# Kernel tuning notes

Hardware: AMD Instinct MI355X
Metric: run time of the kernel (lower is better)

The kernel has to match this reference:

```python
import jax, jax.numpy as jnp
import numpy as np

SRC_K = 11  # source neighborhood
GUI_K = 5   # guide neighborhood


def _unfold(x, k):
    # torch F.unfold(x, k, padding=k//2).view(B, C, k*k, H, W)
    # conv_general_dilated_patches (NCHW default) stacks patches channel-major:
    # output channels ordered (C, kh, kw), matching torch's view.
    p = jax.lax.conv_general_dilated_patches(x, (k, k), (1, 1), 'SAME')
    B, _, H, W = p.shape
    C = x.shape[1]
    return p.reshape(B, C, k * k, H, W)


def _conv1x1(x, w, b):
    # w: (Cout, Cin), 1x1 conv == per-pixel linear
    return jnp.einsum('oi,bihw->bohw', w, x) + b[None, :, None, None]


def setup_inputs() -> dict:
    key = jax.random.key(0)
    ks = jax.random.split(key, 6)
    B, C, H, W = 2, 64, 112, 112
    s1 = 1.0 / np.sqrt(C).astype(np.float32)
    s3 = 1.0 / np.sqrt(2 * C).astype(np.float32)
    return {
        'f_guide': jax.random.normal(ks[0], (B, C, H, W), jnp.float32),
        'f_source': jax.random.normal(ks[1], (B, C, H, W), jnp.float32),
        'w1': jax.random.normal(ks[2], (C, C), jnp.float32) * s1,
        'b1': jnp.zeros((C,), jnp.float32),
        'w2': jax.random.normal(ks[3], (C, C), jnp.float32) * s1,
        'b2': jnp.zeros((C,), jnp.float32),
        'w3': jax.random.normal(ks[4], (C, 2 * C), jnp.float32) * s3,
        'b3': jnp.zeros((C,), jnp.float32),
    }


def reference(f_guide, f_source, w1, b1, w2, b2, w3, b3):
    g = _conv1x1(f_guide, w1, b1)    # (B,C,H,W)
    s = _conv1x1(f_source, w2, b2)   # (B,C,H,W)

    # source -> guide: gather 11x11 source neighborhoods, score vs guide pixel
    fs = _unfold(s, SRC_K)                                   # (B,C,121,H,W)
    filt = jax.nn.softmax((fs * g[:, :, None]).sum(1), 1)    # (B,121,H,W)
    f_s2g = (fs * filt[:, None]).sum(2)                      # (B,C,H,W)

    # guide -> source: gather 5x5 guide neighborhoods, score vs source pixel
    fg = _unfold(g, GUI_K)                                   # (B,C,25,H,W)
    filt2 = jax.nn.softmax((fg * s[:, :, None]).sum(1), 1)   # (B,25,H,W)
    f_g2s = (fg * filt2[:, None]).sum(2)                     # (B,C,H,W)

    fusion = _conv1x1(jnp.concatenate([f_s2g, f_g2s], axis=1), w3, b3)
    return fusion
```

## Files before the change

### kernel.cpp

```cpp
#include <hip/hip_runtime.h>
#include <hip/hip_bf16.h>

constexpr int kH  = 112;
constexpr int kW  = 112;
constexpr int kC  = 64;
constexpr int kB  = 2;
constexpr int kHW = kH * kW;
constexpr int kNP = kB * kHW;

constexpr float kLog2e = 1.4426950408889634f;

__device__ __forceinline__ int xcd1568(int bid) { return (bid & 7) * 196 + (bid >> 3); }
__device__ __forceinline__ int xcd3136(int bid) { return (bid & 7) * 392 + (bid >> 3); }

__global__ __launch_bounds__(256)
void prep(const float* __restrict__ w1, const float* __restrict__ w2,
          const float* __restrict__ w3, float* __restrict__ w1t,
          float* __restrict__ w2t, float* __restrict__ w3t)
{
    const int idx = blockIdx.x * 256 + threadIdx.x;
    if (idx < 4096) {
        const int o = idx >> 6, c = idx & 63;
        w1t[c * 64 + o] = w1[idx];
    } else if (idx < 8192) {
        const int r = idx - 4096;
        const int o = r >> 6, c = r & 63;
        w2t[c * 64 + o] = w2[r];
    } else {
        const int r = idx - 8192;
        const int o = r >> 7, c = r & 127;
        w3t[c * 64 + o] = w3[r];
    }
}

__global__ __launch_bounds__(256, 4)
void conv_gs(const float* __restrict__ fg, const float* __restrict__ fs,
             const float* __restrict__ w1t, const float* __restrict__ b1,
             const float* __restrict__ w2t, const float* __restrict__ b2,
             float* __restrict__ gw, float* __restrict__ sw)
{
    __shared__ float wt[2][4096];
    __shared__ float xls[2][64 * 17];

    for (int idx = threadIdx.x; idx < 8192; idx += 256) {
        const int t = idx >> 12, rem = idx & 4095;
        wt[t][rem] = (t ? w2t : w1t)[rem];
    }

    const int d   = xcd1568(blockIdx.x);
    const int p0  = d * 16;
    const int b   = p0 / kHW;
    const int pb0 = p0 - b * kHW;

    for (int idx = threadIdx.x; idx < 2048; idx += 256) {
        const int t  = idx >> 10;
        const int c  = (idx >> 4) & 63;
        const int px = idx & 15;
        xls[t][c * 17 + px] = (t ? fs : fg)[(size_t)(b * kC + c) * kHW + pb0 + px];
    }
    __syncthreads();

    const int grp = threadIdx.x >> 4;
    const int i   = threadIdx.x & 15;
    const int t   = i >> 3;
    const int j   = i & 7;
    const int p   = p0 + grp;

    float x[8];
#pragma unroll
    for (int cc = 0; cc < 8; ++cc)
        x[cc] = xls[t][(8 * j + cc) * 17 + grp];

    const float* bias = t ? b2 : b1;
    const float* wts  = wt[t];

    float a[8];
    {
        const float4 bb0  = *(const float4*)(bias + 8 * j);
        const float4 bb1v = *(const float4*)(bias + 8 * j + 4);
        a[0] = bb0.x;  a[1] = bb0.y;  a[2] = bb0.z;  a[3] = bb0.w;
        a[4] = bb1v.x; a[5] = bb1v.y; a[6] = bb1v.z; a[7] = bb1v.w;
    }

    for (int c0 = 0; c0 < 64; c0 += 8) {
        const int sl = c0 >> 3;
#pragma unroll
        for (int k = 0; k < 8; ++k) {
            const float xc = __shfl(x[k], sl, 8);
            const float* wr = &wts[(c0 + k) * 64 + 8 * j];
            const float4 w0 = *(const float4*)(wr);
            const float4 w1v = *(const float4*)(wr + 4);
            a[0] = fmaf(w0.x, xc, a[0]);  a[1] = fmaf(w0.y, xc, a[1]);
            a[2] = fmaf(w0.z, xc, a[2]);  a[3] = fmaf(w0.w, xc, a[3]);
            a[4] = fmaf(w1v.x, xc, a[4]); a[5] = fmaf(w1v.y, xc, a[5]);
            a[6] = fmaf(w1v.z, xc, a[6]); a[7] = fmaf(w1v.w, xc, a[7]);
        }
    }
    float* dst = (t ? sw : gw) + (size_t)p * 64 + 8 * j;
    *(float4*)(dst)     = make_float4(a[0], a[1], a[2], a[3]);
    *(float4*)(dst + 4) = make_float4(a[4], a[5], a[6], a[7]);
}

template <int NN, int KD, int RAD, bool GUARD>
__device__ __forceinline__ void attn_phase(const float* __restrict__ base,
                                           const float qs[8], int pb, int h, int w,
                                           int t, int j, float acc[8], float& l)
{
    const float* np;
    bool v0 = true;
    {
        const int q = t / KD, r = t - q * KD;
        int off;
        if (GUARD) {
            const int hh = h + q - RAD, ww = w + r - RAD;
            v0 = ((unsigned)hh < (unsigned)kH) & ((unsigned)ww < (unsigned)kW);
            off = min(max(hh, 0), kH - 1) * kW + min(max(ww, 0), kW - 1);
        } else {
            off = pb + q * kW + r - (RAD * kW + RAD);
        }
        np = base + (size_t)off * 64 + 8 * j;
    }
    float4 n0 = *(const float4*)(np);
    float4 n1 = *(const float4*)(np + 4);

    for (int n = t; n < NN; n += 4) {
        float4 m0, m1;
        bool v1 = true;
        if (n + 4 < NN) {
            const int q = (n + 4) / KD, r = (n + 4) - q * KD;
            int off;
            if (GUARD) {
                const int hh = h + q - RAD, ww = w + r - RAD;
                v1 = ((unsigned)hh < (unsigned)kH) & ((unsigned)ww < (unsigned)kW);
                off = min(max(hh, 0), kH - 1) * kW + min(max(ww, 0), kW - 1);
            } else {
                off = pb + q * kW + r - (RAD * kW + RAD);
            }
            const float* np2 = base + (size_t)off * 64 + 8 * j;
            m0 = *(const float4*)(np2);
            m1 = *(const float4*)(np2 + 4);
        }

        float4 c0 = n0, c1 = n1;
        if (GUARD && !v0) {
            c0 = make_float4(0.f, 0.f, 0.f, 0.f);
            c1 = make_float4(0.f, 0.f, 0.f, 0.f);
        }
        float dd = c0.x * qs[0];
        dd = fmaf(c0.y, qs[1], dd);
        dd = fmaf(c0.z, qs[2], dd);
        dd = fmaf(c0.w, qs[3], dd);
        dd = fmaf(c1.x, qs[4], dd);
        dd = fmaf(c1.y, qs[5], dd);
        dd = fmaf(c1.z, qs[6], dd);
        dd = fmaf(c1.w, qs[7], dd);
        dd += __shfl_xor(dd, 1);
        dd += __shfl_xor(dd, 2);
        dd += __shfl_xor(dd, 4);
        const float pe = __builtin_amdgcn_exp2f(dd);
        l += pe;
        acc[0] = fmaf(pe, c0.x, acc[0]);
        acc[1] = fmaf(pe, c0.y, acc[1]);
        acc[2] = fmaf(pe, c0.z, acc[2]);
        acc[3] = fmaf(pe, c0.w, acc[3]);
        acc[4] = fmaf(pe, c1.x, acc[4]);
        acc[5] = fmaf(pe, c1.y, acc[5]);
        acc[6] = fmaf(pe, c1.z, acc[6]);
        acc[7] = fmaf(pe, c1.w, acc[7]);

        n0 = m0; n1 = m1; v0 = v1;
    }
}

__device__ __forceinline__ void merge4(float acc[8], float& l)
{
    l += __shfl_xor(l, 8);
    l += __shfl_xor(l, 16);
#pragma unroll
    for (int k = 0; k < 8; ++k) {
        acc[k] += __shfl_xor(acc[k], 8);
        acc[k] += __shfl_xor(acc[k], 16);
    }
}

__global__ __launch_bounds__(256, 8)
void attn_fuse(const float* __restrict__ gw, const float* __restrict__ sw,
               const float* __restrict__ w3t, const float* __restrict__ b3,
               float* __restrict__ out)
{
    const int d   = xcd3136(blockIdx.x);
    const int grp = threadIdx.x >> 5;
    const int i   = threadIdx.x & 31;
    const int t   = i >> 3;
    const int j   = i & 7;
    const int p   = d * 8 + grp;

    const int b  = p / kHW;
    const int pb = p - b * kHW;
    const int h  = pb / kW;
    const int w  = pb - h * kW;

    const float* gb = gw + (size_t)b * kHW * 64;
    const float* sb = sw + (size_t)b * kHW * 64;

    float fs2g[8];
    {
        float qs[8];
        const float4 g0 = *(const float4*)(gw + (size_t)p * 64 + 8 * j);
        const float4 g1 = *(const float4*)(gw + (size_t)p * 64 + 8 * j + 4);
        qs[0] = g0.x * kLog2e; qs[1] = g0.y * kLog2e;
        qs[2] = g0.z * kLog2e; qs[3] = g0.w * kLog2e;
        qs[4] = g1.x * kLog2e; qs[5] = g1.y * kLog2e;
        qs[6] = g1.z * kLog2e; qs[7] = g1.w * kLog2e;

        float acc[8] = {0.f, 0.f, 0.f, 0.f, 0.f, 0.f, 0.f, 0.f};
        float l = 0.f;
        if (h >= 5 && h < kH - 5 && w >= 5 && w < kW - 5)
            attn_phase<121, 11, 5, false>(sb, qs, pb, h, w, t, j, acc, l);
        else
            attn_phase<121, 11, 5, true>(sb, qs, pb, h, w, t, j, acc, l);
        merge4(acc, l);
        const float inv = 1.0f / l;
#pragma unroll
        for (int k = 0; k < 8; ++k) fs2g[k] = acc[k] * inv;
    }

    float fg2s[8];
    {
        float qs[8];
        const float4 s0 = *(const float4*)(sw + (size_t)p * 64 + 8 * j);
        const float4 s1 = *(const float4*)(sw + (size_t)p * 64 + 8 * j + 4);
        qs[0] = s0.x * kLog2e; qs[1] = s0.y * kLog2e;
        qs[2] = s0.z * kLog2e; qs[3] = s0.w * kLog2e;
        qs[4] = s1.x * kLog2e; qs[5] = s1.y * kLog2e;
        qs[6] = s1.z * kLog2e; qs[7] = s1.w * kLog2e;

        float acc[8] = {0.f, 0.f, 0.f, 0.f, 0.f, 0.f, 0.f, 0.f};
        float l = 0.f;
        if (h >= 2 && h < kH - 2 && w >= 2 && w < kW - 2)
            attn_phase<25, 5, 2, false>(gb, qs, pb, h, w, t, j, acc, l);
        else
            attn_phase<25, 5, 2, true>(gb, qs, pb, h, w, t, j, acc, l);
        merge4(acc, l);
        const float inv = 1.0f / l;
#pragma unroll
        for (int k = 0; k < 8; ++k) fg2s[k] = acc[k] * inv;
    }

    float xsrc[8];
#pragma unroll
    for (int k = 0; k < 8; ++k) xsrc[k] = (t < 2) ? fs2g[k] : fg2s[k];

    float fo[8] = {0.f, 0.f, 0.f, 0.f, 0.f, 0.f, 0.f, 0.f};
    for (int m0 = 0; m0 < 32; m0 += 8) {
        const int srcl = (((t & 1) << 5) + m0) >> 3;
        const float* wrow = w3t + (size_t)(t * 32 + m0) * 64 + 8 * j;
#pragma unroll
        for (int mm = 0; mm < 8; ++mm) {
            const float xc = __shfl(xsrc[mm], srcl, 8);
            const float4 w0 = *(const float4*)(wrow + mm * 64);
            const float4 w1v = *(const float4*)(wrow + mm * 64 + 4);
            fo[0] = fmaf(w0.x, xc, fo[0]);  fo[1] = fmaf(w0.y, xc, fo[1]);
            fo[2] = fmaf(w0.z, xc, fo[2]);  fo[3] = fmaf(w0.w, xc, fo[3]);
            fo[4] = fmaf(w1v.x, xc, fo[4]); fo[5] = fmaf(w1v.y, xc, fo[5]);
            fo[6] = fmaf(w1v.z, xc, fo[6]); fo[7] = fmaf(w1v.w, xc, fo[7]);
        }
    }
#pragma unroll
    for (int k = 0; k < 8; ++k) {
        fo[k] += __shfl_xor(fo[k], 8);
        fo[k] += __shfl_xor(fo[k], 16);
    }

    const float e0 = (t & 2) ? fo[4] : fo[0];
    const float e1 = (t & 2) ? fo[5] : fo[1];
    const float e2 = (t & 2) ? fo[6] : fo[2];
    const float e3 = (t & 2) ? fo[7] : fo[3];
    const float o0 = (t & 1) ? e2 : e0;
    const float o1 = (t & 1) ? e3 : e1;
    const int c0 = 8 * j + 2 * t;
    const size_t a0 = ((size_t)(b * kC + c0) * kH + h) * kW + w;
    out[a0]       = o0 + b3[c0];
    out[a0 + kHW] = o1 + b3[c0 + 1];
}

extern "C" void kernel_launch(void* const* d_in, const int* in_sizes, int n_in,
                              void* d_out, int out_size, void* d_ws, size_t ws_size,
                              hipStream_t stream)
{
    const float* fg = (const float*)d_in[0];
    const float* fs = (const float*)d_in[1];
    const float* w1 = (const float*)d_in[2];
    const float* b1 = (const float*)d_in[3];
    const float* w2 = (const float*)d_in[4];
    const float* b2 = (const float*)d_in[5];
    const float* w3 = (const float*)d_in[6];
    const float* b3 = (const float*)d_in[7];
    float* outp = (float*)d_out;

    float* gws = (float*)d_ws;
    float* sws = gws + (size_t)kNP * 64;
    float* w3t = sws + (size_t)kNP * 64;
    float* w1t = w3t + 128 * 64;
    float* w2t = w1t + 64 * 64;

    prep<<<64, 256, 0, stream>>>(w1, w2, w3, w1t, w2t, w3t);
    conv_gs<<<1568, 256, 0, stream>>>(fg, fs, w1t, b1, w2t, b2, gws, sws);
    attn_fuse<<<3136, 256, 0, stream>>>(gws, sws, w3t, b3, outp);
}
```

Before: 174.2 us.

## Stage attention neighborhoods in shared-memory tiles and read conv weights from global

```diff
diff --git a/kernel.cpp b/kernel.cpp
--- a/kernel.cpp
+++ b/kernel.cpp
@@ -11,7 +11,6 @@
 constexpr float kLog2e = 1.4426950408889634f;
 
 __device__ __forceinline__ int xcd1568(int bid) { return (bid & 7) * 196 + (bid >> 3); }
-__device__ __forceinline__ int xcd3136(int bid) { return (bid & 7) * 392 + (bid >> 3); }
 
 __global__ __launch_bounds__(256)
 void prep(const float* __restrict__ w1, const float* __restrict__ w2,
@@ -33,19 +32,13 @@
     }
 }
 
-__global__ __launch_bounds__(256, 4)
+__global__ __launch_bounds__(256, 6)
 void conv_gs(const float* __restrict__ fg, const float* __restrict__ fs,
              const float* __restrict__ w1t, const float* __restrict__ b1,
              const float* __restrict__ w2t, const float* __restrict__ b2,
              float* __restrict__ gw, float* __restrict__ sw)
 {
-    __shared__ float wt[2][4096];
     __shared__ float xls[2][64 * 17];
-
-    for (int idx = threadIdx.x; idx < 8192; idx += 256) {
-        const int t = idx >> 12, rem = idx & 4095;
-        wt[t][rem] = (t ? w2t : w1t)[rem];
-    }
 
     const int d   = xcd1568(blockIdx.x);
     const int p0  = d * 16;
@@ -72,7 +65,7 @@
         x[cc] = xls[t][(8 * j + cc) * 17 + grp];
 
     const float* bias = t ? b2 : b1;
-    const float* wts  = wt[t];
+    const float* wb   = t ? w2t : w1t;
 
     float a[8];
     {
@@ -87,7 +80,7 @@
 #pragma unroll
         for (int k = 0; k < 8; ++k) {
             const float xc = __shfl(x[k], sl, 8);
-            const float* wr = &wts[(c0 + k) * 64 + 8 * j];
+            const float* wr = wb + (c0 + k) * 64 + 8 * j;
             const float4 w0 = *(const float4*)(wr);
             const float4 w1v = *(const float4*)(wr + 4);
             a[0] = fmaf(w0.x, xc, a[0]);  a[1] = fmaf(w0.y, xc, a[1]);
@@ -101,107 +94,44 @@
     *(float4*)(dst + 4) = make_float4(a[4], a[5], a[6], a[7]);
 }
 
-template <int NN, int KD, int RAD, bool GUARD>
-__device__ __forceinline__ void attn_phase(const float* __restrict__ base,
-                                           const float qs[8], int pb, int h, int w,
-                                           int t, int j, float acc[8], float& l)
-{
-    const float* np;
-    bool v0 = true;
-    {
-        const int q = t / KD, r = t - q * KD;
-        int off;
-        if (GUARD) {
-            const int hh = h + q - RAD, ww = w + r - RAD;
-            v0 = ((unsigned)hh < (unsigned)kH) & ((unsigned)ww < (unsigned)kW);
-            off = min(max(hh, 0), kH - 1) * kW + min(max(ww, 0), kW - 1);
-        } else {
-            off = pb + q * kW + r - (RAD * kW + RAD);
-        }
-        np = base + (size_t)off * 64 + 8 * j;
-    }
-    float4 n0 = *(const float4*)(np);
-    float4 n1 = *(const float4*)(np + 4);
-
-    for (int n = t; n < NN; n += 4) {
-        float4 m0, m1;
-        bool v1 = true;
-        if (n + 4 < NN) {
-            const int q = (n + 4) / KD, r = (n + 4) - q * KD;
-            int off;
-            if (GUARD) {
-                const int hh = h + q - RAD, ww = w + r - RAD;
-                v1 = ((unsigned)hh < (unsigned)kH) & ((unsigned)ww < (unsigned)kW);
-                off = min(max(hh, 0), kH - 1) * kW + min(max(ww, 0), kW - 1);
-            } else {
-                off = pb + q * kW + r - (RAD * kW + RAD);
-            }
-            const float* np2 = base + (size_t)off * 64 + 8 * j;
-            m0 = *(const float4*)(np2);
-            m1 = *(const float4*)(np2 + 4);
-        }
-
-        float4 c0 = n0, c1 = n1;
-        if (GUARD && !v0) {
-            c0 = make_float4(0.f, 0.f, 0.f, 0.f);
-            c1 = make_float4(0.f, 0.f, 0.f, 0.f);
-        }
-        float dd = c0.x * qs[0];
-        dd = fmaf(c0.y, qs[1], dd);
-        dd = fmaf(c0.z, qs[2], dd);
-        dd = fmaf(c0.w, qs[3], dd);
-        dd = fmaf(c1.x, qs[4], dd);
-        dd = fmaf(c1.y, qs[5], dd);
-        dd = fmaf(c1.z, qs[6], dd);
-        dd = fmaf(c1.w, qs[7], dd);
-        dd += __shfl_xor(dd, 1);
-        dd += __shfl_xor(dd, 2);
-        dd += __shfl_xor(dd, 4);
-        const float pe = __builtin_amdgcn_exp2f(dd);
-        l += pe;
-        acc[0] = fmaf(pe, c0.x, acc[0]);
-        acc[1] = fmaf(pe, c0.y, acc[1]);
-        acc[2] = fmaf(pe, c0.z, acc[2]);
-        acc[3] = fmaf(pe, c0.w, acc[3]);
-        acc[4] = fmaf(pe, c1.x, acc[4]);
-        acc[5] = fmaf(pe, c1.y, acc[5]);
-        acc[6] = fmaf(pe, c1.z, acc[6]);
-        acc[7] = fmaf(pe, c1.w, acc[7]);
-
-        n0 = m0; n1 = m1; v0 = v1;
-    }
-}
-
-__device__ __forceinline__ void merge4(float acc[8], float& l)
-{
-    l += __shfl_xor(l, 8);
-    l += __shfl_xor(l, 16);
-#pragma unroll
-    for (int k = 0; k < 8; ++k) {
-        acc[k] += __shfl_xor(acc[k], 8);
-        acc[k] += __shfl_xor(acc[k], 16);
-    }
-}
-
-__global__ __launch_bounds__(256, 8)
+constexpr int kSP = 68;
+
+__global__ __launch_bounds__(512, 4)
 void attn_fuse(const float* __restrict__ gw, const float* __restrict__ sw,
                const float* __restrict__ w3t, const float* __restrict__ b3,
                float* __restrict__ out)
 {
-    const int d   = xcd3136(blockIdx.x);
+    __shared__ float tile[216 * kSP];
+
+    const int d    = xcd1568(blockIdx.x);
+    const int b    = d / 784;
+    const int r    = d - b * 784;
+    const int band = r / 14;
+    const int tw   = r - band * 14;
+    const int h0   = band * 2;
+    const int w0   = tw * 8;
+
     const int grp = threadIdx.x >> 5;
     const int i   = threadIdx.x & 31;
     const int t   = i >> 3;
     const int j   = i & 7;
-    const int p   = d * 8 + grp;
-
-    const int b  = p / kHW;
-    const int pb = p - b * kHW;
-    const int h  = pb / kW;
-    const int w  = pb - h * kW;
+    const int ly  = grp >> 3;
+    const int lx  = grp & 7;
+    const int h   = h0 + ly;
+    const int w   = w0 + lx;
+    const int p   = (b * kH + h) * kW + w;
 
     const float* gb = gw + (size_t)b * kHW * 64;
     const float* sb = sw + (size_t)b * kHW * 64;
+
+    for (int idx = threadIdx.x; idx < 216 * 64; idx += 512) {
+        const int pix = idx >> 6, c = idx & 63;
+        const int py = pix / 18, px = pix - py * 18;
+        const int gh = h0 - 5 + py, gx = w0 - 5 + px;
+        const bool v = ((unsigned)gh < (unsigned)kH) & ((unsigned)gx < (unsigned)kW);
+        tile[pix * kSP + c] = v ? sb[(size_t)(gh * kW + gx) * 64 + c] : 0.f;
+    }
+    __syncthreads();
 
     float fs2g[8];
     {
@@ -215,15 +145,54 @@
 
         float acc[8] = {0.f, 0.f, 0.f, 0.f, 0.f, 0.f, 0.f, 0.f};
         float l = 0.f;
-        if (h >= 5 && h < kH - 5 && w >= 5 && w < kW - 5)
-            attn_phase<121, 11, 5, false>(sb, qs, pb, h, w, t, j, acc, l);
-        else
-            attn_phase<121, 11, 5, true>(sb, qs, pb, h, w, t, j, acc, l);
-        merge4(acc, l);
+        for (int n = t; n < 121; n += 4) {
+            const int q = n / 11, rr = n - q * 11;
+            const float* np = &tile[((ly + q) * 18 + lx + rr) * kSP + 8 * j];
+            const float4 n0 = *(const float4*)(np);
+            const float4 n1 = *(const float4*)(np + 4);
+            float dd = n0.x * qs[0];
+            dd = fmaf(n0.y, qs[1], dd);
+            dd = fmaf(n0.z, qs[2], dd);
+            dd = fmaf(n0.w, qs[3], dd);
+            dd = fmaf(n1.x, qs[4], dd);
+            dd = fmaf(n1.y, qs[5], dd);
+            dd = fmaf(n1.z, qs[6], dd);
+            dd = fmaf(n1.w, qs[7], dd);
+            dd += __shfl_xor(dd, 1);
+            dd += __shfl_xor(dd, 2);
+            dd += __shfl_xor(dd, 4);
+            const float pe = __builtin_amdgcn_exp2f(dd);
+            l += pe;
+            acc[0] = fmaf(pe, n0.x, acc[0]);
+            acc[1] = fmaf(pe, n0.y, acc[1]);
+            acc[2] = fmaf(pe, n0.z, acc[2]);
+            acc[3] = fmaf(pe, n0.w, acc[3]);
+            acc[4] = fmaf(pe, n1.x, acc[4]);
+            acc[5] = fmaf(pe, n1.y, acc[5]);
+            acc[6] = fmaf(pe, n1.z, acc[6]);
+            acc[7] = fmaf(pe, n1.w, acc[7]);
+        }
+        l += __shfl_xor(l, 8);
+        l += __shfl_xor(l, 16);
+#pragma unroll
+        for (int k = 0; k < 8; ++k) {
+            acc[k] += __shfl_xor(acc[k], 8);
+            acc[k] += __shfl_xor(acc[k], 16);
+        }
         const float inv = 1.0f / l;
 #pragma unroll
         for (int k = 0; k < 8; ++k) fs2g[k] = acc[k] * inv;
     }
+    __syncthreads();
+
+    for (int idx = threadIdx.x; idx < 72 * 64; idx += 512) {
+        const int pix = idx >> 6, c = idx & 63;
+        const int py = pix / 12, px = pix - py * 12;
+        const int gh = h0 - 2 + py, gx = w0 - 2 + px;
+        const bool v = ((unsigned)gh < (unsigned)kH) & ((unsigned)gx < (unsigned)kW);
+        tile[pix * kSP + c] = v ? gb[(size_t)(gh * kW + gx) * 64 + c] : 0.f;
+    }
+    __syncthreads();
 
     float fg2s[8];
     {
@@ -237,11 +206,40 @@
 
         float acc[8] = {0.f, 0.f, 0.f, 0.f, 0.f, 0.f, 0.f, 0.f};
         float l = 0.f;
-        if (h >= 2 && h < kH - 2 && w >= 2 && w < kW - 2)
-            attn_phase<25, 5, 2, false>(gb, qs, pb, h, w, t, j, acc, l);
-        else
-            attn_phase<25, 5, 2, true>(gb, qs, pb, h, w, t, j, acc, l);
-        merge4(acc, l);
+        for (int n = t; n < 25; n += 4) {
+            const int q = n / 5, rr = n - q * 5;
+            const float* np = &tile[((ly + q) * 12 + lx + rr) * kSP + 8 * j];
+            const float4 n0 = *(const float4*)(np);
+            const float4 n1 = *(const float4*)(np + 4);
+            float dd = n0.x * qs[0];
+            dd = fmaf(n0.y, qs[1], dd);
+            dd = fmaf(n0.z, qs[2], dd);
+            dd = fmaf(n0.w, qs[3], dd);
+            dd = fmaf(n1.x, qs[4], dd);
+            dd = fmaf(n1.y, qs[5], dd);
+            dd = fmaf(n1.z, qs[6], dd);
+            dd = fmaf(n1.w, qs[7], dd);
+            dd += __shfl_xor(dd, 1);
+            dd += __shfl_xor(dd, 2);
+            dd += __shfl_xor(dd, 4);
+            const float pe = __builtin_amdgcn_exp2f(dd);
+            l += pe;
+            acc[0] = fmaf(pe, n0.x, acc[0]);
+            acc[1] = fmaf(pe, n0.y, acc[1]);
+            acc[2] = fmaf(pe, n0.z, acc[2]);
+            acc[3] = fmaf(pe, n0.w, acc[3]);
+            acc[4] = fmaf(pe, n1.x, acc[4]);
+            acc[5] = fmaf(pe, n1.y, acc[5]);
+            acc[6] = fmaf(pe, n1.z, acc[6]);
+            acc[7] = fmaf(pe, n1.w, acc[7]);
+        }
+        l += __shfl_xor(l, 8);
+        l += __shfl_xor(l, 16);
+#pragma unroll
+        for (int k = 0; k < 8; ++k) {
+            acc[k] += __shfl_xor(acc[k], 8);
+            acc[k] += __shfl_xor(acc[k], 16);
+        }
         const float inv = 1.0f / l;
 #pragma unroll
         for (int k = 0; k < 8; ++k) fg2s[k] = acc[k] * inv;
@@ -306,5 +304,5 @@
 
     prep<<<64, 256, 0, stream>>>(w1, w2, w3, w1t, w2t, w3t);
     conv_gs<<<1568, 256, 0, stream>>>(fg, fs, w1t, b1, w2t, b2, gws, sws);
-    attn_fuse<<<3136, 256, 0, stream>>>(gws, sws, w3t, b3, outp);
+    attn_fuse<<<1568, 512, 0, stream>>>(gws, sws, w3t, b3, outp);
 }
```

After: 199.6 us. 1.15x slower.
